# Optimization experiments

Hardware: AMD Instinct MI355X
Metric: run time of the kernel (lower is better)

## Reference

```python
import jax, jax.numpy as jnp
import numpy as np

N = 100000   # nodes
E = 1600000  # edges
G = 512      # graphs
EPS_MSG = 1e-7   # GENConv message eps
EPS_SM = 1e-16   # PyG softmax denom eps
BN_EPS = 1e-5    # BatchNorm eps (eval mode, running mean=0, var=1)


def setup_inputs() -> dict:
    key = jax.random.key(0)
    ks = iter(jax.random.split(key, 40))
    d = {}
    d['x'] = jax.random.normal(next(ks), (N, 10), dtype=jnp.float32)
    d['edge_index'] = jax.random.randint(next(ks), (2, E), 0, N, dtype=jnp.int64)
    d['batch'] = jax.random.randint(next(ks), (N,), 0, G, dtype=jnp.int64)

    def lin(k, fo, fi):
        k1, k2 = jax.random.split(k)
        s = 1.0 / np.sqrt(fi)
        return (jax.random.uniform(k1, (fo, fi), jnp.float32, -s, s),
                jax.random.uniform(k2, (fo,), jnp.float32, -s, s))

    # conv1: lin_src/lin_dst 10->100, MLP [100,200,100] with BN(200)
    d['c1_src_w'], d['c1_src_b'] = lin(next(ks), 100, 10)
    d['c1_dst_w'], d['c1_dst_b'] = lin(next(ks), 100, 10)
    d['c1_w1'], d['c1_b1'] = lin(next(ks), 200, 100)
    d['c1_g'] = jnp.ones((200,), jnp.float32)
    d['c1_be'] = jnp.zeros((200,), jnp.float32)
    d['c1_w2'], d['c1_b2'] = lin(next(ks), 100, 200)
    # conv2 / conv3: in==out -> no lin_src/dst; MLP [100,200,100]
    for p in ('c2', 'c3'):
        d[p + '_w1'], d[p + '_b1'] = lin(next(ks), 200, 100)
        d[p + '_g'] = jnp.ones((200,), jnp.float32)
        d[p + '_be'] = jnp.zeros((200,), jnp.float32)
        d[p + '_w2'], d[p + '_b2'] = lin(next(ks), 100, 200)
    d['fc1_w'], d['fc1_b'] = lin(next(ks), 100, 200)
    d['cls_w'], d['cls_b'] = lin(next(ks), 2, 100)
    return d


def _genconv(x, src, dst, src_w, src_b, dst_w, dst_b, w1, b1, g, be, w2, b2):
    # GENConv, aggr='softmax', t=1, eval-mode BN in MLP
    h = x if src_w is None else x @ src_w.T + src_b          # [N, 100]
    msg = jax.nn.relu(h[src]) + EPS_MSG                       # [E, 100]
    m = jax.ops.segment_max(msg, dst, num_segments=N)
    m = jnp.where(jnp.isfinite(m), m, 0.0)
    e = jnp.exp(msg - m[dst])
    den = jax.ops.segment_sum(e, dst, num_segments=N)
    alpha = e / (den[dst] + EPS_SM)
    agg = jax.ops.segment_sum(alpha * msg, dst, num_segments=N)  # [N, 100]
    xd = x if dst_w is None else x @ dst_w.T + dst_b
    out = agg + xd
    # MLP: Linear -> BN(eval: mean0,var1) -> ReLU -> Linear
    hh = out @ w1.T + b1
    hh = hh * (g / np.sqrt(1.0 + BN_EPS)) + be
    hh = jax.nn.relu(hh)
    return hh @ w2.T + b2


def _readout(x, batch):
    s = jax.ops.segment_sum(x, batch, num_segments=G)
    cnt = jax.ops.segment_sum(jnp.ones((x.shape[0],), x.dtype), batch, num_segments=G)
    mean = s / jnp.maximum(cnt, 1.0)[:, None]
    mx = jax.ops.segment_max(x, batch, num_segments=G)
    mx = jnp.where(jnp.isfinite(mx), mx, 0.0)
    return jnp.concatenate([mean, mx], axis=-1)  # [G, 200]


def reference(x, edge_index, batch,
              c1_src_w, c1_src_b, c1_dst_w, c1_dst_b, c1_w1, c1_b1, c1_g, c1_be, c1_w2, c1_b2,
              c2_w1, c2_b1, c2_g, c2_be, c2_w2, c2_b2,
              c3_w1, c3_b1, c3_g, c3_be, c3_w2, c3_b2,
              fc1_w, fc1_b, cls_w, cls_b):
    src, dst = edge_index[0], edge_index[1]
    h = jax.nn.relu(_genconv(x, src, dst, c1_src_w, c1_src_b, c1_dst_w, c1_dst_b,
                             c1_w1, c1_b1, c1_g, c1_be, c1_w2, c1_b2))
    x1 = _readout(h, batch)
    h = jax.nn.relu(_genconv(h, src, dst, None, None, None, None,
                             c2_w1, c2_b1, c2_g, c2_be, c2_w2, c2_b2))
    x2 = _readout(h, batch)
    h = jax.nn.relu(_genconv(h, src, dst, None, None, None, None,
                             c3_w1, c3_b1, c3_g, c3_be, c3_w2, c3_b2))
    x3 = _readout(h, batch)
    encode = jax.nn.relu(x1) + jax.nn.relu(x2) + jax.nn.relu(x3)  # [G, 200]
    z = jax.nn.relu(encode @ fc1_w.T + fc1_b)  # dropout is identity in eval
    logits = z @ cls_w.T + cls_b               # [G, 2]
    return (logits, encode)
```

## Files before the change

### kernel.cpp

```cpp
#include <hip/hip_runtime.h>
#include <cstdint>
#include <cstddef>

#define XF 10
#define NF 100
#define HF 200
#define BSHIFT 8
#define NBLK_G 512
#define MAXBK 512
#define RCH 4

typedef _Float16 f16x8 __attribute__((ext_vector_type(8)));
typedef _Float16 h2 __attribute__((ext_vector_type(2)));
typedef float f32x4 __attribute__((ext_vector_type(4)));

static __device__ __forceinline__ float bn_scale(float g) {
    return g * 0.9999950000374997f;
}

__global__ __launch_bounds__(256) void csr_count_kernel(const int* __restrict__ eidx,
                                                        int* __restrict__ bmat,
                                                        int E, int nbk, int epb) {
    __shared__ int hist[MAXBK];
    for (int j = threadIdx.x; j < nbk; j += 256) hist[j] = 0;
    __syncthreads();
    int base = blockIdx.x * epb;
    int end = base + epb; if (end > E) end = E;
    for (int e = base + threadIdx.x; e < end; e += 256) {
        int d = eidx[E + e];
        atomicAdd(&hist[d >> BSHIFT], 1);
    }
    __syncthreads();
    for (int j = threadIdx.x; j < nbk; j += 256)
        bmat[(size_t)j * NBLK_G + blockIdx.x] = hist[j];
}

__global__ __launch_bounds__(256) void scan1x_kernel(int* __restrict__ a,
                                                     int* __restrict__ blocksum, int n) {
    __shared__ int s[256];
    int t = threadIdx.x;
    int base = blockIdx.x * 1024 + t * 4;
    int v[4]; int tot = 0;
#pragma unroll
    for (int i = 0; i < 4; ++i) {
        v[i] = (base + i < n) ? a[base + i] : 0;
        tot += v[i];
    }
    s[t] = tot;
    __syncthreads();
    for (int off = 1; off < 256; off <<= 1) {
        int add = (t >= off) ? s[t - off] : 0;
        __syncthreads();
        s[t] += add;
        __syncthreads();
    }
    int run = s[t] - tot;
#pragma unroll
    for (int i = 0; i < 4; ++i) {
        if (base + i < n) a[base + i] = run;
        run += v[i];
    }
    if (t == 255) blocksum[blockIdx.x] = s[255];
}

__global__ void small_scan_kernel(const int* __restrict__ in, int in_stride,
                                  int* __restrict__ cur, int cur_stride,
                                  int* __restrict__ indptr, int n) {
    __shared__ int s[256];
    int t = threadIdx.x;
    int base = t * 4;
    int v[4]; int tot = 0;
#pragma unroll
    for (int i = 0; i < 4; ++i) {
        v[i] = (base + i < n) ? in[(base + i) * in_stride] : 0;
        tot += v[i];
    }
    s[t] = tot;
    __syncthreads();
    for (int off = 1; off < 256; off <<= 1) {
        int add = (t >= off) ? s[t - off] : 0;
        __syncthreads();
        s[t] += add;
        __syncthreads();
    }
    int run = s[t] - tot;
#pragma unroll
    for (int i = 0; i < 4; ++i) {
        if (base + i < n) {
            cur[(base + i) * cur_stride] = run;
            run += v[i];
            if (indptr) indptr[base + i + 1] = run;
        }
    }
    if (t == 0 && indptr) indptr[0] = 0;
}

__global__ __launch_bounds__(256) void csr_scatter_kernel(const int* __restrict__ eidx,
                                                          const int* __restrict__ bmat,
                                                          const int* __restrict__ blocksum,
                                                          int* __restrict__ packed,
                                                          int E, int nbk, int epb) {
    __shared__ int cur[MAXBK];
    for (int j = threadIdx.x; j < nbk; j += 256) {
        size_t idx = (size_t)j * NBLK_G + blockIdx.x;
        cur[j] = bmat[idx] + blocksum[idx >> 10];
    }
    __syncthreads();
    int base = blockIdx.x * epb;
    int end = base + epb; if (end > E) end = E;
    for (int e = base + threadIdx.x; e < end; e += 256) {
        int s = eidx[e];
        int d = eidx[E + e];
        int p = atomicAdd(&cur[d >> BSHIFT], 1);
        packed[p] = s | ((d & 255) << 24);
    }
}

__global__ __launch_bounds__(256) void csr_finalize_kernel(const int* __restrict__ bmat,
                                                           const int* __restrict__ blocksum,
                                                           const int* __restrict__ packed,
                                                           int* __restrict__ indptr,
                                                           int* __restrict__ esrc,
                                                           int E, int nbk, int n) {
    __shared__ int cnt[256];
    __shared__ int s[256];
    __shared__ int cur[256];
    int b = blockIdx.x;
    int t = threadIdx.x;
    size_t i0 = (size_t)b * NBLK_G;
    int ebeg = bmat[i0] + blocksum[i0 >> 10];
    int eend = E;
    if (b + 1 < nbk) {
        size_t i1 = (size_t)(b + 1) * NBLK_G;
        eend = bmat[i1] + blocksum[i1 >> 10];
    }
    cnt[t] = 0;
    __syncthreads();
    for (int i = ebeg + t; i < eend; i += 256)
        atomicAdd(&cnt[((unsigned)packed[i]) >> 24], 1);
    __syncthreads();
    int tot = cnt[t];
    s[t] = tot;
    __syncthreads();
    for (int off = 1; off < 256; off <<= 1) {
        int add = (t >= off) ? s[t - off] : 0;
        __syncthreads();
        s[t] += add;
        __syncthreads();
    }
    int off_ex = s[t] - tot;
    int node = (b << BSHIFT) + t;
    if (node < n) indptr[node] = ebeg + off_ex;
    if (b == nbk - 1 && t == 0) indptr[n] = E;
    cur[t] = ebeg + off_ex;
    __syncthreads();
    for (int i = ebeg + t; i < eend; i += 256) {
        int p = packed[i];
        int pos = atomicAdd(&cur[((unsigned)p) >> 24], 1);
        esrc[pos] = p & 0xFFFFFF;
    }
}

__global__ __launch_bounds__(256) void gcnt_kernel(const int* __restrict__ batch,
                                                   int* __restrict__ gcount, int n) {
    int i = blockIdx.x * 256 + threadIdx.x;
    if (i < n) atomicAdd(&gcount[batch[i]], 1);
}

__global__ __launch_bounds__(256) void gfill_kernel(const int* __restrict__ batch,
                                                    int* __restrict__ gcur,
                                                    int* __restrict__ gnodes, int n) {
    int i = blockIdx.x * 256 + threadIdx.x;
    if (i >= n) return;
    int g = batch[i];
    int p = atomicAdd(&gcur[g], 1);
    gnodes[p] = i;
}

struct WArgs {
    const float* src[6];
    _Float16* dst[6];
};
__global__ __launch_bounds__(256) void wconv_kernel(WArgs wa) {
    int w = blockIdx.y;
    int idx = blockIdx.x * 256 + threadIdx.x;
    int J, K, j, k;
    if (w < 3) { J = 200; K = 100; j = idx >> 7; k = idx & 127; }
    else       { J = 100; K = 200; j = idx >> 8; k = idx & 255; }
    float v = (j < J && k < K) ? wa.src[w][j * K + k] : 0.f;
    wa.dst[w][idx] = (_Float16)v;
}

__global__ __launch_bounds__(256) void lin10_kernel(const float* __restrict__ x,
                                                    const float* __restrict__ sw,
                                                    const float* __restrict__ sb,
                                                    const float* __restrict__ dw,
                                                    const float* __restrict__ db,
                                                    _Float16* __restrict__ h16,
                                                    _Float16* __restrict__ xd16, int n_nodes) {
    int idx = blockIdx.x * 256 + threadIdx.x;
    if (idx >= n_nodes * 64) return;
    int n = idx >> 6, f2 = idx & 63;
    float a0 = 0.f, a1 = 0.f, b0 = 0.f, b1 = 0.f;
    if (f2 < 50) {
        int f0 = 2 * f2, f1 = 2 * f2 + 1;
        float xv[XF];
#pragma unroll
        for (int k = 0; k < XF; ++k) xv[k] = x[n * XF + k];
        a0 = sb[f0]; a1 = sb[f1]; b0 = db[f0]; b1 = db[f1];
#pragma unroll
        for (int k = 0; k < XF; ++k) {
            a0 += xv[k] * sw[f0 * XF + k];
            a1 += xv[k] * sw[f1 * XF + k];
            b0 += xv[k] * dw[f0 * XF + k];
            b1 += xv[k] * dw[f1 * XF + k];
        }
    }
    ((h2*)(h16 + (size_t)n * 128))[f2] = (h2){(_Float16)a0, (_Float16)a1};
    ((h2*)(xd16 + (size_t)n * 128))[f2] = (h2){(_Float16)b0, (_Float16)b1};
}

__global__ __launch_bounds__(128) void agg_kernel(const _Float16* __restrict__ h16,
                                                  const _Float16* __restrict__ xd16,
                                                  const int* __restrict__ indptr,
                                                  const int* __restrict__ esrc,
                                                  _Float16* __restrict__ c16, int n_nodes) {
    int n = blockIdx.x * 2 + (threadIdx.x >> 6);
    if (n >= n_nodes) return;
    int lane = threadIdx.x & 63;
    int beg = __builtin_amdgcn_readfirstlane(indptr[n]);
    int end = __builtin_amdgcn_readfirstlane(indptr[n + 1]);
    int deg = end - beg;
    const h2* hb = (const h2*)h16;
    float d0 = 0.f, d1 = 0.f, s0 = 0.f, s1 = 0.f;
    const float L2E = 1.44269504088896f;
    h2 va[4], vb[4];
    if (deg > 0) {
#pragma unroll
        for (int k = 0; k < 4; ++k) {
            int j = (k < deg) ? k : deg - 1;
            unsigned sidx = (unsigned)esrc[beg + j];
            va[k] = hb[(size_t)sidx * 64 + lane];
        }
    }
    for (int r = 0; r < deg; r += 4) {
        if (r + 4 < deg) {
#pragma unroll
            for (int k = 0; k < 4; ++k) {
                int j = (r + 4 + k < deg) ? r + 4 + k : deg - 1;
                unsigned sidx = (unsigned)esrc[beg + j];
                vb[k] = hb[(size_t)sidx * 64 + lane];
            }
        }
        int km = deg - r; if (km > 4) km = 4;
#pragma unroll
        for (int k = 0; k < 4; ++k) {
            if (k < km) {
                float a0 = fmaxf((float)va[k].x, 0.f) + 1e-7f;
                float a1 = fmaxf((float)va[k].y, 0.f) + 1e-7f;
                float e0 = __builtin_amdgcn_exp2f(fmaf(a0, L2E, -40.f));
                float e1 = __builtin_amdgcn_exp2f(fmaf(a1, L2E, -40.f));
                d0 += e0; s0 = fmaf(e0, a0, s0);
                d1 += e1; s1 = fmaf(e1, a1, s1);
            }
        }
#pragma unroll
        for (int k = 0; k < 4; ++k) va[k] = vb[k];
    }
    const float EPS = 9.094947e-29f;
    float g0 = s0 / (d0 + EPS);
    float g1 = s1 / (d1 + EPS);
    float o0 = 0.f, o1 = 0.f;
    if (lane < 50) {
        h2 xv = ((const h2*)(xd16 + (size_t)n * 128))[lane];
        o0 = g0 + (float)xv.x;
        o1 = g1 + (float)xv.y;
    }
    ((h2*)(c16 + (size_t)n * 128))[lane] = (h2){(_Float16)o0, (_Float16)o1};
}

__global__ __launch_bounds__(256, 3) void mlp_fused_kernel(const _Float16* __restrict__ A,
                                                           const _Float16* __restrict__ W1,
                                                           const float* __restrict__ b1v,
                                                           const float* __restrict__ g1v,
                                                           const float* __restrict__ be1v,
                                                           const _Float16* __restrict__ W2,
                                                           const float* __restrict__ b2v,
                                                           _Float16* __restrict__ out16,
                                                           int M) {
    __shared__ _Float16 hh[64][264];
    int wave = threadIdx.x >> 6;
    int lane = threadIdx.x & 63;
    int l15 = lane & 15, quad = lane >> 4;
    long m0 = (long)blockIdx.x * 64;

    const _Float16* aptr = A + (m0 + l15) * 128 + quad * 8;
    const _Float16* w1p  = W1 + (size_t)(wave * 64 + l15) * 128 + quad * 8;
    f32x4 acc[4][4] = {};
#pragma unroll 2
    for (int ks = 0; ks < 4; ++ks) {
        f16x8 bfr[4], afr[4];
#pragma unroll
        for (int ct = 0; ct < 4; ++ct) bfr[ct] = *(const f16x8*)(w1p + (size_t)ct * 16 * 128 + ks * 32);
#pragma unroll
        for (int i = 0; i < 4; ++i) afr[i] = *(const f16x8*)(aptr + (size_t)i * 16 * 128 + ks * 32);
#pragma unroll
        for (int i = 0; i < 4; ++i)
#pragma unroll
            for (int ct = 0; ct < 4; ++ct)
                acc[i][ct] = __builtin_amdgcn_mfma_f32_16x16x32_f16(afr[i], bfr[ct], acc[i][ct], 0, 0, 0);
    }
#pragma unroll
    for (int ct = 0; ct < 4; ++ct) {
        int col = wave * 64 + ct * 16 + l15;
        bool cv = col < HF;
        float bi = cv ? b1v[col] : 0.f;
        float gm = cv ? bn_scale(g1v[col]) : 0.f;
        float bt = cv ? be1v[col] : 0.f;
#pragma unroll
        for (int i = 0; i < 4; ++i)
#pragma unroll
            for (int r = 0; r < 4; ++r) {
                float v = fmaxf((acc[i][ct][r] + bi) * gm + bt, 0.f);
                hh[i * 16 + quad * 4 + r][col] = (_Float16)v;
            }
    }
    __syncthreads();

    const _Float16* w2p = W2 + (size_t)(wave * 32 + l15) * 256 + quad * 8;
    f32x4 o[4][2] = {};
#pragma unroll 2
    for (int ks = 0; ks < 8; ++ks) {
        f16x8 bfr[2], afr[4];
#pragma unroll
        for (int ct = 0; ct < 2; ++ct) bfr[ct] = *(const f16x8*)(w2p + (size_t)ct * 16 * 256 + ks * 32);
#pragma unroll
        for (int i = 0; i < 4; ++i) afr[i] = *(const f16x8*)(&hh[i * 16 + l15][quad * 8 + ks * 32]);
#pragma unroll
        for (int i = 0; i < 4; ++i)
#pragma unroll
            for (int ct = 0; ct < 2; ++ct)
                o[i][ct] = __builtin_amdgcn_mfma_f32_16x16x32_f16(afr[i], bfr[ct], o[i][ct], 0, 0, 0);
    }
#pragma unroll
    for (int ct = 0; ct < 2; ++ct) {
        int col = wave * 32 + ct * 16 + l15;
        bool cv = col < NF;
        float bi = cv ? b2v[col] : 0.f;
#pragma unroll
        for (int i = 0; i < 4; ++i)
#pragma unroll
            for (int r = 0; r < 4; ++r) {
                long row = m0 + i * 16 + quad * 4 + r;
                float v = fmaxf(o[i][ct][r] + bi, 0.f);
                if (!cv) v = 0.f;
                if (row < M) out16[row * 128 + col] = (_Float16)v;
            }
    }
}

__global__ __launch_bounds__(256) void readout2_kernel(const _Float16* __restrict__ h16,
                                                       const int* __restrict__ gindptr,
                                                       const int* __restrict__ gnodes,
                                                       float* __restrict__ sumpart,
                                                       float* __restrict__ maxpart, int G) {
    __shared__ float ls[4][128];
    __shared__ float lm[4][128];
    int g = blockIdx.x, ch = blockIdx.y;
    int wave = threadIdx.x >> 6;
    int lane = threadIdx.x & 63;
    int beg = gindptr[g], end = gindptr[g + 1];
    const h2* hb = (const h2*)h16;
    float s0 = 0.f, s1 = 0.f, m0 = 0.f, m1 = 0.f;
    int i = beg + ch * 4 + wave;
    int nd = (i < end) ? gnodes[i] : 0;
    for (; i < end; i += 16) {
        int ndn = (i + 16 < end) ? gnodes[i + 16] : 0;
        h2 v = hb[(size_t)nd * 64 + lane];
        float v0 = (float)v.x, v1 = (float)v.y;
        s0 += v0; s1 += v1;
        m0 = fmaxf(m0, v0); m1 = fmaxf(m1, v1);
        nd = ndn;
    }
    ls[wave][2 * lane] = s0; ls[wave][2 * lane + 1] = s1;
    lm[wave][2 * lane] = m0; lm[wave][2 * lane + 1] = m1;
    __syncthreads();
    int f = threadIdx.x;
    if (f < NF) {
        float ss = ls[0][f] + ls[1][f] + ls[2][f] + ls[3][f];
        float mm = fmaxf(fmaxf(lm[0][f], lm[1][f]), fmaxf(lm[2][f], lm[3][f]));
        sumpart[((size_t)ch * G + g) * NF + f] = ss;
        maxpart[((size_t)ch * G + g) * NF + f] = mm;
    }
}

__global__ __launch_bounds__(256) void head_kernel(const float* __restrict__ rbuf,
                                                   const int* __restrict__ gindptr,
                                                   const float* __restrict__ fc1w,
                                                   const float* __restrict__ fc1b,
                                                   const float* __restrict__ clsw,
                                                   const float* __restrict__ clsb,
                                                   float* __restrict__ out, int G) {
    __shared__ float enc[HF];
    __shared__ float z[NF];
    int g = blockIdx.x;
    int t = threadIdx.x;
    float ic = 1.f / fmaxf((float)(gindptr[g + 1] - gindptr[g]), 1.f);
    if (t < HF) {
        float e = 0.f;
        if (t < NF) {
#pragma unroll
            for (int l = 0; l < 3; ++l) {
                float s = 0.f;
#pragma unroll
                for (int ch = 0; ch < RCH; ++ch)
                    s += rbuf[(((size_t)(l * 2) * RCH + ch) * G + g) * NF + t];
                e += fmaxf(s * ic, 0.f);
            }
        } else {
            int f = t - NF;
#pragma unroll
            for (int l = 0; l < 3; ++l) {
                float mm = 0.f;
#pragma unroll
                for (int ch = 0; ch < RCH; ++ch)
                    mm = fmaxf(mm, rbuf[(((size_t)(l * 2 + 1) * RCH + ch) * G + g) * NF + f]);
                e += fmaxf(mm, 0.f);
            }
        }
        enc[t] = e;
        out[G * 2 + (size_t)g * HF + t] = e;
    }
    __syncthreads();
    if (t < NF) {
        float a = fc1b[t];
        for (int k = 0; k < HF; ++k) a += enc[k] * fc1w[t * HF + k];
        z[t] = fmaxf(a, 0.f);
    }
    __syncthreads();
    if (t < 2) {
        float a = clsb[t];
        for (int k = 0; k < NF; ++k) a += z[k] * clsw[t * NF + k];
        out[(size_t)g * 2 + t] = a;
    }
}

extern "C" void kernel_launch(void* const* d_in, const int* in_sizes, int n_in,
                              void* d_out, int out_size, void* d_ws, size_t ws_size,
                              hipStream_t stream) {
    const float* x        = (const float*)d_in[0];
    const int*   eidx     = (const int*)d_in[1];
    const int*   batch    = (const int*)d_in[2];
    const float* c1_src_w = (const float*)d_in[3];
    const float* c1_src_b = (const float*)d_in[4];
    const float* c1_dst_w = (const float*)d_in[5];
    const float* c1_dst_b = (const float*)d_in[6];
    const float* cw1[3] = {(const float*)d_in[7],  (const float*)d_in[13], (const float*)d_in[19]};
    const float* cb1[3] = {(const float*)d_in[8],  (const float*)d_in[14], (const float*)d_in[20]};
    const float* cg[3]  = {(const float*)d_in[9],  (const float*)d_in[15], (const float*)d_in[21]};
    const float* cbe[3] = {(const float*)d_in[10], (const float*)d_in[16], (const float*)d_in[22]};
    const float* cw2[3] = {(const float*)d_in[11], (const float*)d_in[17], (const float*)d_in[23]};
    const float* cb2[3] = {(const float*)d_in[12], (const float*)d_in[18], (const float*)d_in[24]};
    const float* fc1w = (const float*)d_in[25];
    const float* fc1b = (const float*)d_in[26];
    const float* clsw = (const float*)d_in[27];
    const float* clsb = (const float*)d_in[28];

    const int N = in_sizes[0] / XF;
    const int E = in_sizes[1] / 2;
    const int G = out_size / 202;
    const int Mpad = (N + 63) & ~63;
    const int NBK = (N + 255) >> BSHIFT;
    const int EPB = (E + NBLK_G - 1) / NBLK_G;
    const int BM = NBK * NBLK_G;
    const int NB2 = (BM + 1023) / 1024;

    char* p = (char*)d_ws;
    auto alloc = [&](size_t bytes) {
        char* r = p;
        p += (bytes + 255) & ~(size_t)255;
        return r;
    };
    _Float16* h16  = (_Float16*)alloc((size_t)Mpad * 128 * 2);
    _Float16* C16  = (_Float16*)alloc((size_t)Mpad * 128 * 2);
    _Float16* xd16 = (_Float16*)alloc((size_t)Mpad * 128 * 2);
    _Float16* W16  = (_Float16*)alloc((size_t)6 * 32768 * 2);
    int* packed   = (int*)alloc((size_t)E * 4);
    int* esrc     = (int*)alloc((size_t)E * 4);
    int* indptr   = (int*)alloc((size_t)(N + 1) * 4);
    int* bmat     = (int*)alloc((size_t)BM * 4);
    int* blocksum = (int*)alloc((size_t)NB2 * 4);
    int* gcount   = (int*)alloc((size_t)G * 4);
    int* gcur     = (int*)alloc((size_t)G * 4);
    int* gindptr  = (int*)alloc((size_t)(G + 1) * 4);
    int* gnodes   = (int*)alloc((size_t)N * 4);
    float* rbuf   = (float*)alloc((size_t)6 * RCH * G * NF * 4);

    (void)hipMemsetAsync(gcount, 0, (size_t)G * 4, stream);

    csr_count_kernel<<<NBLK_G, 256, 0, stream>>>(eidx, bmat, E, NBK, EPB);
    scan1x_kernel<<<NB2, 256, 0, stream>>>(bmat, blocksum, BM);
    small_scan_kernel<<<1, 256, 0, stream>>>(blocksum, 1, blocksum, 1, nullptr, NB2);
    csr_scatter_kernel<<<NBLK_G, 256, 0, stream>>>(eidx, bmat, blocksum, packed, E, NBK, EPB);
    csr_finalize_kernel<<<NBK, 256, 0, stream>>>(bmat, blocksum, packed, indptr, esrc, E, NBK, N);

    gcnt_kernel<<<(N + 255) / 256, 256, 0, stream>>>(batch, gcount, N);
    small_scan_kernel<<<1, 256, 0, stream>>>(gcount, 1, gcur, 1, gindptr, G);
    gfill_kernel<<<(N + 255) / 256, 256, 0, stream>>>(batch, gcur, gnodes, N);

    WArgs wa;
    for (int l = 0; l < 3; ++l) {
        wa.src[l] = cw1[l];     wa.dst[l] = W16 + (size_t)l * 32768;
        wa.src[3 + l] = cw2[l]; wa.dst[3 + l] = W16 + (size_t)(3 + l) * 32768;
    }
    wconv_kernel<<<dim3(128, 6), 256, 0, stream>>>(wa);

    lin10_kernel<<<((size_t)N * 64 + 255) / 256, 256, 0, stream>>>(x, c1_src_w, c1_src_b,
                                                                   c1_dst_w, c1_dst_b, h16, xd16, N);

    for (int l = 0; l < 3; ++l) {
        const _Float16* xdp = (l == 0) ? xd16 : h16;
        agg_kernel<<<(N + 1) / 2, 128, 0, stream>>>(h16, xdp, indptr, esrc, C16, N);
        mlp_fused_kernel<<<Mpad / 64, 256, 0, stream>>>(
            C16, W16 + (size_t)l * 32768, cb1[l], cg[l], cbe[l],
            W16 + (size_t)(3 + l) * 32768, cb2[l], h16, N);
        readout2_kernel<<<dim3(G, RCH), 256, 0, stream>>>(
            h16, gindptr, gnodes,
            rbuf + (size_t)(l * 2) * RCH * G * NF,
            rbuf + (size_t)(l * 2 + 1) * RCH * G * NF, G);
    }

    head_kernel<<<G, 256, 0, stream>>>(rbuf, gindptr, fc1w, fc1b, clsw, clsb, (float*)d_out, G);
    (void)ws_size;
}
```

Measured before the change: 684.3 us.

## Fuse softmax aggregation into MLP kernel via shared-memory staging

Merges the per-node softmax aggregation and the two-layer MLP into one kernel. Each 64-row block first gathers neighbor features and builds its aggregated input tile in LDS, then runs the MFMA MLP straight from LDS, so the intermediate C16 buffer is never written to or read from global memory. The h buffers are ping-ponged because the layer now reads and writes node features in the same launch. The cost is much less gather parallelism: each wave handles 16 nodes one after another, against 50k small blocks before, and the extra LDS may lower occupancy, so gather latency may be hidden less well.

```diff
diff --git a/kernel.cpp b/kernel.cpp
--- a/kernel.cpp
+++ b/kernel.cpp
@@ -220,82 +220,82 @@
     ((h2*)(xd16 + (size_t)n * 128))[f2] = (h2){(_Float16)b0, (_Float16)b1};
 }
 
-__global__ __launch_bounds__(128) void agg_kernel(const _Float16* __restrict__ h16,
-                                                  const _Float16* __restrict__ xd16,
-                                                  const int* __restrict__ indptr,
-                                                  const int* __restrict__ esrc,
-                                                  _Float16* __restrict__ c16, int n_nodes) {
-    int n = blockIdx.x * 2 + (threadIdx.x >> 6);
-    if (n >= n_nodes) return;
-    int lane = threadIdx.x & 63;
-    int beg = __builtin_amdgcn_readfirstlane(indptr[n]);
-    int end = __builtin_amdgcn_readfirstlane(indptr[n + 1]);
-    int deg = end - beg;
-    const h2* hb = (const h2*)h16;
-    float d0 = 0.f, d1 = 0.f, s0 = 0.f, s1 = 0.f;
-    const float L2E = 1.44269504088896f;
-    h2 va[4], vb[4];
-    if (deg > 0) {
-#pragma unroll
-        for (int k = 0; k < 4; ++k) {
-            int j = (k < deg) ? k : deg - 1;
-            unsigned sidx = (unsigned)esrc[beg + j];
-            va[k] = hb[(size_t)sidx * 64 + lane];
-        }
-    }
-    for (int r = 0; r < deg; r += 4) {
-        if (r + 4 < deg) {
-#pragma unroll
-            for (int k = 0; k < 4; ++k) {
-                int j = (r + 4 + k < deg) ? r + 4 + k : deg - 1;
-                unsigned sidx = (unsigned)esrc[beg + j];
-                vb[k] = hb[(size_t)sidx * 64 + lane];
-            }
-        }
-        int km = deg - r; if (km > 4) km = 4;
-#pragma unroll
-        for (int k = 0; k < 4; ++k) {
-            if (k < km) {
-                float a0 = fmaxf((float)va[k].x, 0.f) + 1e-7f;
-                float a1 = fmaxf((float)va[k].y, 0.f) + 1e-7f;
-                float e0 = __builtin_amdgcn_exp2f(fmaf(a0, L2E, -40.f));
-                float e1 = __builtin_amdgcn_exp2f(fmaf(a1, L2E, -40.f));
-                d0 += e0; s0 = fmaf(e0, a0, s0);
-                d1 += e1; s1 = fmaf(e1, a1, s1);
-            }
-        }
-#pragma unroll
-        for (int k = 0; k < 4; ++k) va[k] = vb[k];
-    }
-    const float EPS = 9.094947e-29f;
-    float g0 = s0 / (d0 + EPS);
-    float g1 = s1 / (d1 + EPS);
-    float o0 = 0.f, o1 = 0.f;
-    if (lane < 50) {
-        h2 xv = ((const h2*)(xd16 + (size_t)n * 128))[lane];
-        o0 = g0 + (float)xv.x;
-        o1 = g1 + (float)xv.y;
-    }
-    ((h2*)(c16 + (size_t)n * 128))[lane] = (h2){(_Float16)o0, (_Float16)o1};
-}
-
-__global__ __launch_bounds__(256, 3) void mlp_fused_kernel(const _Float16* __restrict__ A,
-                                                           const _Float16* __restrict__ W1,
-                                                           const float* __restrict__ b1v,
-                                                           const float* __restrict__ g1v,
-                                                           const float* __restrict__ be1v,
-                                                           const _Float16* __restrict__ W2,
-                                                           const float* __restrict__ b2v,
-                                                           _Float16* __restrict__ out16,
-                                                           int M) {
+__global__ __launch_bounds__(256, 3) void layer_fused_kernel(const _Float16* __restrict__ hin,
+                                                             const _Float16* __restrict__ xd,
+                                                             const int* __restrict__ indptr,
+                                                             const int* __restrict__ esrc,
+                                                             const _Float16* __restrict__ W1,
+                                                             const float* __restrict__ b1v,
+                                                             const float* __restrict__ g1v,
+                                                             const float* __restrict__ be1v,
+                                                             const _Float16* __restrict__ W2,
+                                                             const float* __restrict__ b2v,
+                                                             _Float16* __restrict__ out16,
+                                                             int M) {
+    __shared__ _Float16 ain[64][136];
     __shared__ _Float16 hh[64][264];
     int wave = threadIdx.x >> 6;
     int lane = threadIdx.x & 63;
     int l15 = lane & 15, quad = lane >> 4;
     long m0 = (long)blockIdx.x * 64;
-
-    const _Float16* aptr = A + (m0 + l15) * 128 + quad * 8;
-    const _Float16* w1p  = W1 + (size_t)(wave * 64 + l15) * 128 + quad * 8;
+    const h2* hb = (const h2*)hin;
+    const float L2E = 1.44269504088896f;
+    const float EPS = 9.094947e-29f;
+
+    for (int i = 0; i < 16; ++i) {
+        int n = (int)m0 + wave * 16 + i;
+        float o0 = 0.f, o1 = 0.f;
+        if (n < M) {
+            int beg = __builtin_amdgcn_readfirstlane(indptr[n]);
+            int end = __builtin_amdgcn_readfirstlane(indptr[n + 1]);
+            int deg = end - beg;
+            float d0 = 0.f, d1 = 0.f, s0 = 0.f, s1 = 0.f;
+            h2 va[4], vb[4];
+            if (deg > 0) {
+#pragma unroll
+                for (int k = 0; k < 4; ++k) {
+                    int j = (k < deg) ? k : deg - 1;
+                    unsigned sidx = (unsigned)esrc[beg + j];
+                    va[k] = hb[(size_t)sidx * 64 + lane];
+                }
+            }
+            for (int r = 0; r < deg; r += 4) {
+                if (r + 4 < deg) {
+#pragma unroll
+                    for (int k = 0; k < 4; ++k) {
+                        int j = (r + 4 + k < deg) ? r + 4 + k : deg - 1;
+                        unsigned sidx = (unsigned)esrc[beg + j];
+                        vb[k] = hb[(size_t)sidx * 64 + lane];
+                    }
+                }
+                int km = deg - r; if (km > 4) km = 4;
+#pragma unroll
+                for (int k = 0; k < 4; ++k) {
+                    if (k < km) {
+                        float a0 = fmaxf((float)va[k].x, 0.f) + 1e-7f;
+                        float a1 = fmaxf((float)va[k].y, 0.f) + 1e-7f;
+                        float e0 = __builtin_amdgcn_exp2f(fmaf(a0, L2E, -40.f));
+                        float e1 = __builtin_amdgcn_exp2f(fmaf(a1, L2E, -40.f));
+                        d0 += e0; s0 = fmaf(e0, a0, s0);
+                        d1 += e1; s1 = fmaf(e1, a1, s1);
+                    }
+                }
+#pragma unroll
+                for (int k = 0; k < 4; ++k) va[k] = vb[k];
+            }
+            float g0 = s0 / (d0 + EPS);
+            float g1 = s1 / (d1 + EPS);
+            if (lane < 50) {
+                h2 xv = ((const h2*)(xd + (size_t)n * 128))[lane];
+                o0 = g0 + (float)xv.x;
+                o1 = g1 + (float)xv.y;
+            }
+        }
+        ((h2*)(&ain[wave * 16 + i][0]))[lane] = (h2){(_Float16)o0, (_Float16)o1};
+    }
+    __syncthreads();
+
+    const _Float16* w1p = W1 + (size_t)(wave * 64 + l15) * 128 + quad * 8;
     f32x4 acc[4][4] = {};
 #pragma unroll 2
     for (int ks = 0; ks < 4; ++ks) {
@@ -303,7 +303,7 @@
 #pragma unroll
         for (int ct = 0; ct < 4; ++ct) bfr[ct] = *(const f16x8*)(w1p + (size_t)ct * 16 * 128 + ks * 32);
 #pragma unroll
-        for (int i = 0; i < 4; ++i) afr[i] = *(const f16x8*)(aptr + (size_t)i * 16 * 128 + ks * 32);
+        for (int i = 0; i < 4; ++i) afr[i] = *(const f16x8*)(&ain[i * 16 + l15][ks * 32 + quad * 8]);
 #pragma unroll
         for (int i = 0; i < 4; ++i)
 #pragma unroll
@@ -481,8 +481,8 @@
         p += (bytes + 255) & ~(size_t)255;
         return r;
     };
-    _Float16* h16  = (_Float16*)alloc((size_t)Mpad * 128 * 2);
-    _Float16* C16  = (_Float16*)alloc((size_t)Mpad * 128 * 2);
+    _Float16* hA   = (_Float16*)alloc((size_t)Mpad * 128 * 2);
+    _Float16* hB   = (_Float16*)alloc((size_t)Mpad * 128 * 2);
     _Float16* xd16 = (_Float16*)alloc((size_t)Mpad * 128 * 2);
     _Float16* W16  = (_Float16*)alloc((size_t)6 * 32768 * 2);
     int* packed   = (int*)alloc((size_t)E * 4);
@@ -516,16 +516,18 @@
     wconv_kernel<<<dim3(128, 6), 256, 0, stream>>>(wa);
 
     lin10_kernel<<<((size_t)N * 64 + 255) / 256, 256, 0, stream>>>(x, c1_src_w, c1_src_b,
-                                                                   c1_dst_w, c1_dst_b, h16, xd16, N);
-
+                                                                   c1_dst_w, c1_dst_b, hA, xd16, N);
+
+    const _Float16* hin[3] = {hA, hB, hA};
+    _Float16* hout[3]      = {hB, hA, hB};
     for (int l = 0; l < 3; ++l) {
-        const _Float16* xdp = (l == 0) ? xd16 : h16;
-        agg_kernel<<<(N + 1) / 2, 128, 0, stream>>>(h16, xdp, indptr, esrc, C16, N);
-        mlp_fused_kernel<<<Mpad / 64, 256, 0, stream>>>(
-            C16, W16 + (size_t)l * 32768, cb1[l], cg[l], cbe[l],
-            W16 + (size_t)(3 + l) * 32768, cb2[l], h16, N);
+        const _Float16* xdp = (l == 0) ? xd16 : hin[l];
+        layer_fused_kernel<<<Mpad / 64, 256, 0, stream>>>(
+            hin[l], xdp, indptr, esrc,
+            W16 + (size_t)l * 32768, cb1[l], cg[l], cbe[l],
+            W16 + (size_t)(3 + l) * 32768, cb2[l], hout[l], N);
         readout2_kernel<<<dim3(G, RCH), 256, 0, stream>>>(
-            h16, gindptr, gnodes,
+            hout[l], gindptr, gnodes,
             rbuf + (size_t)(l * 2) * RCH * G * NF,
             rbuf + (size_t)(l * 2 + 1) * RCH * G * NF, G);
     }
```

Result: slower. 891.9 us (+30.3%).
